# Optimization experiments

Measured on AMD Instinct MI355X. Metric: run time of the kernel, lower is better.

Reference implementation:

```python
import jax, jax.numpy as jnp
import numpy as np
import math

NO, NR, E = 100000, 1000, 1000000
DO, DR, DE, H, OM = 64, 32, 4, 64, 32


def setup_inputs() -> dict:
    key = jax.random.key(0)
    ks = jax.random.split(key, 20)
    s = lambda k, sh: jax.random.normal(k, sh, dtype=jnp.float32) * 0.05
    inp = {
        'x_order': jax.random.normal(ks[0], (NO, DO), dtype=jnp.float32),
        'x_rider': jax.random.normal(ks[1], (NR, DR), dtype=jnp.float32),
        'edge_attr': jax.random.normal(ks[2], (E, DE), dtype=jnp.float32),
        'order_idx': jax.random.randint(ks[3], (E,), 0, NO),
        'rider_idx': jax.random.randint(ks[4], (E,), 0, NR),
        'omega_encoded': jax.random.normal(ks[5], (OM,), dtype=jnp.float32),
        # TransformerConv params (heads=1)
        'Wk': s(ks[6], (DO, H)), 'bk': jnp.zeros((H,), jnp.float32),
        'Wq': s(ks[7], (DR, H)), 'bq': jnp.zeros((H,), jnp.float32),
        'Wv': s(ks[8], (DO, H)), 'bv': jnp.zeros((H,), jnp.float32),
        'We': s(ks[9], (DE, H)),  # lin_edge, bias=False in PyG
        'Wskip': s(ks[10], (DR, H)), 'bskip': jnp.zeros((H,), jnp.float32),
        # order_proj
        'Wp': s(ks[11], (DO, H)), 'bp': jnp.zeros((H,), jnp.float32),
        # residual MLP: Linear(2H+OM,128) -> ReLU -> Linear(128,1)
        'W1': s(ks[12], (2 * H + OM, 128)), 'b1': jnp.zeros((128,), jnp.float32),
        'W2': s(ks[13], (128, 1)), 'b2': jnp.zeros((1,), jnp.float32),
    }
    return inp


def _segment_softmax(alpha, seg, num_segments):
    m = jax.ops.segment_max(alpha, seg, num_segments=num_segments)
    m = jnp.where(jnp.isfinite(m), m, 0.0)
    ex = jnp.exp(alpha - m[seg])
    denom = jax.ops.segment_sum(ex, seg, num_segments=num_segments)
    return ex / (denom[seg] + 1e-16)


def reference(x_order, x_rider, edge_attr, order_idx, rider_idx, omega_encoded,
              Wk, bk, Wq, bq, Wv, bv, We, Wskip, bskip, Wp, bp, W1, b1, W2, b2):
    scale = 1.0 / math.sqrt(H)
    # TransformerConv((order, rider) -> rider), heads=1, edge_dim
    q = x_rider @ Wq + bq            # [NR, H]
    k = x_order @ Wk + bk            # [NO, H]
    v = x_order @ Wv + bv            # [NO, H]
    e = edge_attr @ We               # [E, H]
    k_j = k[order_idx] + e           # [E, H]
    v_j = v[order_idx] + e           # [E, H]
    alpha = jnp.sum(q[rider_idx] * k_j, axis=-1) * scale  # [E]
    alpha = _segment_softmax(alpha, rider_idx, NR)
    agg = jax.ops.segment_sum(alpha[:, None] * v_j, rider_idx, num_segments=NR)  # [NR, H]
    rider_emb = agg + x_rider @ Wskip + bskip  # root/skip connection

    # edge scoring
    order_proj = x_order @ Wp + bp   # [NO, H]
    oe = order_proj[order_idx]       # [E, H]
    re = rider_emb[rider_idx]        # [E, H]
    dot = jnp.sum(oe * re, axis=-1) * scale  # [E]
    omega_expand = jnp.broadcast_to(omega_encoded[None, :], (oe.shape[0], OM))
    resid_in = jnp.concatenate([oe, re, omega_expand], axis=-1)  # [E, 2H+OM]
    hmid = jax.nn.relu(resid_in @ W1 + b1)
    resid = (hmid @ W2 + b2)[:, 0]
    return jnp.clip(dot + resid, -10.0, 10.0)
```

## Files before the change

kernel.cpp:

```cpp
#include <hip/hip_runtime.h>
#include <hip/hip_bf16.h>
#include <math.h>
#include <stdint.h>

#define NO_N 100000
#define NR_N 1000
#define E_N  1000000
#define SB     250
#define SCHUNK 4000
#define KVP_TILES 1563
#define KVP_BLKS 1024
#define MAXTILES 17008

typedef short bf16x8 __attribute__((ext_vector_type(8)));
typedef float floatx4 __attribute__((ext_vector_type(4)));

__device__ __forceinline__ unsigned short bfu(float x) {
    union { __hip_bfloat16 h; unsigned short u; } c;
    c.h = __float2bfloat16(x);
    return c.u;
}
__device__ __forceinline__ float bflo(unsigned int u) {
    return __uint_as_float(u << 16);
}
__device__ __forceinline__ float bfhi(unsigned int u) {
    return __uint_as_float(u & 0xffff0000u);
}

__global__ __launch_bounds__(256) void k_front(
    const float* __restrict__ xr,
    const float* __restrict__ Wq, const float* __restrict__ bq,
    const float* __restrict__ Wskip, const float* __restrict__ bskip,
    const float* __restrict__ We,
    float* __restrict__ q, float* __restrict__ skip, float* __restrict__ t,
    const float* __restrict__ W1, const float* __restrict__ b1,
    const float* __restrict__ omega, float* __restrict__ b1eff,
    const float* __restrict__ x,
    const float* __restrict__ Wk, const float* __restrict__ bk,
    const float* __restrict__ Wv, const float* __restrict__ bv,
    const float* __restrict__ Wp, const float* __restrict__ bp,
    unsigned short* __restrict__ kb, unsigned short* __restrict__ vb,
    unsigned short* __restrict__ pb,
    const int* __restrict__ ridx, int* __restrict__ ghist)
{
    __shared__ __align__(16) char smem[9216];
    const int tid = threadIdx.x;
    const int b = blockIdx.x;

    if (b < 250) {
        float* sx = (float*)smem;
        float* sq = sx + 128;
        int rbase = b * 4;
        if (tid < 128) {
            int rl = tid >> 5, d = tid & 31;
            sx[rl * 32 + d] = xr[(rbase + rl) * 32 + d];
        }
        __syncthreads();
        int rl = tid >> 6, h = tid & 63;
        int r = rbase + rl;
        float aq = bq[h], as = bskip[h];
        #pragma unroll 4
        for (int d = 0; d < 32; ++d) {
            float xv = sx[rl * 32 + d];
            aq += xv * Wq[d * 64 + h];
            as += xv * Wskip[d * 64 + h];
        }
        sq[rl * 64 + h] = aq;
        q[r * 64 + h] = aq;
        skip[r * 64 + h] = as;
        __syncthreads();
        if (tid < 16) {
            int rl2 = tid >> 2, d = tid & 3;
            float acc = 0.f;
            for (int hh = 0; hh < 64; ++hh)
                acc += We[d * 64 + hh] * sq[rl2 * 64 + hh];
            t[(rbase + rl2) * 4 + d] = acc;
        }
    } else if (b == 250) {
        if (tid < 128) {
            float acc = b1[tid];
            #pragma unroll 4
            for (int j = 0; j < 32; ++j)
                acc += omega[j] * W1[(128 + j) * 128 + tid];
            b1eff[tid] = acc;
        }
    } else if (b < 251 + KVP_BLKS) {
        unsigned short* sX = (unsigned short*)smem;
        const int wave = tid >> 6, lane = tid & 63;
        const int l15 = lane & 15, quad = lane >> 4;

        bf16x8 bfr[3][2];
        float bias[3];
        unsigned short* outT[3];
        int colc[3];
        #pragma unroll
        for (int ct = 0; ct < 3; ++ct) {
            int n = wave * 48 + ct * 16 + l15;
            int table = n >> 6, c = n & 63;
            const float* W  = (table == 0) ? Wk : (table == 1) ? Wv : Wp;
            const float* bb = (table == 0) ? bk : (table == 1) ? bv : bp;
            bias[ct] = bb[c];
            colc[ct] = c;
            outT[ct] = (table == 0) ? kb : (table == 1) ? vb : pb;
            #pragma unroll
            for (int kf = 0; kf < 2; ++kf) {
                bf16x8 f;
                #pragma unroll
                for (int j = 0; j < 8; ++j)
                    f[j] = (short)bfu(W[(size_t)(kf * 32 + quad * 8 + j) * 64 + c]);
                bfr[ct][kf] = f;
            }
        }

        const int srl = tid >> 2;
        const int sqt = (tid & 3) * 16;

        for (int tile = b - 251; tile < KVP_TILES; tile += KVP_BLKS) {
            int rowbase = tile * 64;
            {
                int row = rowbase + srl;
                unsigned short* dst = sX + srl * 72 + sqt;
                if (row < NO_N) {
                    const float4* src = (const float4*)(x + (size_t)row * 64 + sqt);
                    #pragma unroll
                    for (int i = 0; i < 4; ++i) {
                        float4 a = src[i];
                        ushort4 u = { bfu(a.x), bfu(a.y), bfu(a.z), bfu(a.w) };
                        *(ushort4*)(dst + i * 4) = u;
                    }
                } else {
                    ushort4 z = {0, 0, 0, 0};
                    #pragma unroll
                    for (int i = 0; i < 4; ++i) *(ushort4*)(dst + i * 4) = z;
                }
            }
            __syncthreads();

            floatx4 acc[4][3];
            #pragma unroll
            for (int rt = 0; rt < 4; ++rt)
                #pragma unroll
                for (int ct = 0; ct < 3; ++ct)
                    acc[rt][ct] = (floatx4){bias[ct], bias[ct], bias[ct], bias[ct]};

            #pragma unroll
            for (int rt = 0; rt < 4; ++rt) {
                const unsigned short* ar = sX + (size_t)(rt * 16 + l15) * 72 + quad * 8;
                bf16x8 a0 = *(const bf16x8*)(ar);
                bf16x8 a1 = *(const bf16x8*)(ar + 32);
                #pragma unroll
                for (int ct = 0; ct < 3; ++ct) {
                    floatx4 c = acc[rt][ct];
                    c = __builtin_amdgcn_mfma_f32_16x16x32_bf16(a0, bfr[ct][0], c, 0, 0, 0);
                    c = __builtin_amdgcn_mfma_f32_16x16x32_bf16(a1, bfr[ct][1], c, 0, 0, 0);
                    acc[rt][ct] = c;
                }
            }

            #pragma unroll
            for (int rt = 0; rt < 4; ++rt) {
                int rb = rowbase + rt * 16 + quad * 4;
                #pragma unroll
                for (int ct = 0; ct < 3; ++ct) {
                    unsigned short* o = outT[ct];
                    size_t cbase = colc[ct];
                    #pragma unroll
                    for (int g = 0; g < 4; ++g) {
                        int row = rb + g;
                        if (row < NO_N)
                            o[(size_t)row * 64 + cbase] = bfu(acc[rt][ct][g]);
                    }
                }
            }
            __syncthreads();
        }
    } else {
        int* hc = (int*)smem;
        int hb = b - (251 + KVP_BLKS);
        for (int i = tid; i < NR_N; i += 256) hc[i] = 0;
        __syncthreads();
        int s = hb * SCHUNK;
        for (int i = s + tid; i < s + SCHUNK; i += 256)
            atomicAdd(&hc[ridx[i]], 1);
        __syncthreads();
        for (int i = tid; i < NR_N; i += 256)
            ghist[i * SB + hb] = hc[i];
    }
}

__global__ __launch_bounds__(256) void k_colscan(const int* __restrict__ ghist,
                                                 int* __restrict__ gpre,
                                                 int* __restrict__ counts)
{
    __shared__ int s[256];
    int tid = threadIdx.x, r = blockIdx.x;
    int v = (tid < SB) ? ghist[r * SB + tid] : 0;
    s[tid] = v;
    __syncthreads();
    for (int off = 1; off < 256; off <<= 1) {
        int tv = (tid >= off) ? s[tid - off] : 0;
        __syncthreads();
        s[tid] += tv;
        __syncthreads();
    }
    if (tid < SB) gpre[r * SB + tid] = s[tid] - v;
    if (tid == 255) counts[r] = s[255];
}

__global__ __launch_bounds__(1024) void k_scan(const int* __restrict__ counts,
                                               int* __restrict__ offsets,
                                               int* __restrict__ tilestart,
                                               int4* __restrict__ trec)
{
    __shared__ int s[1024];
    int tid = threadIdx.x;
    int c = (tid < NR_N) ? counts[tid] : 0;
    s[tid] = c;
    __syncthreads();
    for (int off = 1; off < 1024; off <<= 1) {
        int tv = (tid >= off) ? s[tid - off] : 0;
        __syncthreads();
        s[tid] += tv;
        __syncthreads();
    }
    int off0 = s[tid] - c;
    if (tid < NR_N) offsets[tid] = off0;
    if (tid == NR_N - 1) offsets[NR_N] = s[tid];
    __syncthreads();
    int tc = (tid < NR_N) ? ((c + 63) >> 6) : 0;
    s[tid] = tc;
    __syncthreads();
    for (int off = 1; off < 1024; off <<= 1) {
        int tv = (tid >= off) ? s[tid - off] : 0;
        __syncthreads();
        s[tid] += tv;
        __syncthreads();
    }
    if (tid < NR_N) {
        int ts = s[tid] - tc;
        tilestart[tid] = ts;
        int jend = off0 + c;
        for (int t = 0; t < tc; ++t)
            trec[ts + t] = make_int4(tid, off0 + (t << 6), jend, 0);
    }
    if (tid == NR_N - 1) tilestart[NR_N] = s[tid];
}

__global__ __launch_bounds__(256) void k_scatter2(
    const int* __restrict__ ridx, const int* __restrict__ oidx,
    const float* __restrict__ ea, const float* __restrict__ t,
    const int* __restrict__ offsets, const int* __restrict__ gpre,
    int4* __restrict__ spack, int* __restrict__ so, int* __restrict__ rank)
{
    __shared__ int cur[NR_N];
    int tid = threadIdx.x, b = blockIdx.x;
    for (int i = tid; i < NR_N; i += 256)
        cur[i] = offsets[i] + gpre[i * SB + b];
    __syncthreads();
    int s = b * SCHUNK;
    for (int i = s + tid; i < s + SCHUNK; i += 256) {
        int r = ridx[i];
        int o = oidx[i];
        float4 e4 = *(const float4*)(ea + (size_t)i * 4);
        float4 t4 = *(const float4*)(t + r * 4);
        float h = e4.x * t4.x + e4.y * t4.y + e4.z * t4.z + e4.w * t4.w;
        int pos = atomicAdd(&cur[r], 1);
        int4 pk;
        pk.x = o;
        pk.y = __float_as_int(h);
        pk.z = (int)((unsigned)bfu(e4.x) | ((unsigned)bfu(e4.y) << 16));
        pk.w = (int)((unsigned)bfu(e4.z) | ((unsigned)bfu(e4.w) << 16));
        spack[pos] = pk;
        so[pos] = o;
        rank[i] = pos;
    }
}

__global__ __launch_bounds__(512) void k_rider(
    const int* __restrict__ offsets, const int4* __restrict__ spack,
    const float* __restrict__ q,
    const unsigned short* __restrict__ kb, const unsigned short* __restrict__ vb,
    const float* __restrict__ We, const float* __restrict__ skip,
    const float* __restrict__ W1, const float* __restrict__ b1eff,
    float* __restrict__ emb, float* __restrict__ Br)
{
    __shared__ float sQ[64];
    __shared__ int2 sOX[8][64];
    __shared__ float rv[8][64];
    __shared__ float re4[8][4];
    __shared__ float rd[8];

    int r = blockIdx.x;
    int wave = threadIdx.x >> 6, lane = threadIdx.x & 63;
    if (threadIdx.x < 64) sQ[threadIdx.x] = q[r * 64 + threadIdx.x];
    __syncthreads();

    int beg = offsets[r], end = offsets[r + 1];
    int cnt = end - beg;
    int chunk = (cnt + 7) >> 3;
    int s0 = beg + wave * chunk;
    int s1 = min(s0 + chunk, end);

    float aggv = 0.f, dsum = 0.f;
    float ag0 = 0.f, ag1 = 0.f, ag2 = 0.f, ag3 = 0.f;
    const float2* sQ2 = (const float2*)sQ;

    for (int jb = s0; jb < s1; jb += 64) {
        int j = jb + lane;
        bool valid = (j < s1);
        int4 pk = make_int4(0, 0, 0, 0);
        if (valid) pk = spack[j];
        int oo = pk.x;
        float h = __int_as_float(pk.y);

        const uint4* krow = (const uint4*)(kb + (size_t)oo * 64);
        uint4 K0 = krow[0], K1 = krow[1], K2 = krow[2], K3 = krow[3];
        uint4 K4 = krow[4], K5 = krow[5], K6 = krow[6], K7 = krow[7];
        float acc = h;
        #define DOT8(Kv, base) { \
            float2 qa = sQ2[(base) + 0]; \
            acc = fmaf(bflo(Kv.x), qa.x, acc); acc = fmaf(bfhi(Kv.x), qa.y, acc); \
            float2 qb = sQ2[(base) + 1]; \
            acc = fmaf(bflo(Kv.y), qb.x, acc); acc = fmaf(bfhi(Kv.y), qb.y, acc); \
            float2 qc = sQ2[(base) + 2]; \
            acc = fmaf(bflo(Kv.z), qc.x, acc); acc = fmaf(bfhi(Kv.z), qc.y, acc); \
            float2 qd = sQ2[(base) + 3]; \
            acc = fmaf(bflo(Kv.w), qd.x, acc); acc = fmaf(bfhi(Kv.w), qd.y, acc); }
        DOT8(K0, 0) DOT8(K1, 4) DOT8(K2, 8) DOT8(K3, 12)
        DOT8(K4, 16) DOT8(K5, 20) DOT8(K6, 24) DOT8(K7, 28)
        #undef DOT8

        float exv = valid ? __expf(acc * 0.125f) : 0.f;
        dsum += exv;
        unsigned int ez = (unsigned int)pk.z, ew = (unsigned int)pk.w;
        ag0 = fmaf(exv, bflo(ez), ag0);
        ag1 = fmaf(exv, bfhi(ez), ag1);
        ag2 = fmaf(exv, bflo(ew), ag2);
        ag3 = fmaf(exv, bfhi(ew), ag3);

        sOX[wave][lane] = make_int2(oo, __float_as_int(exv));

        int nn = min(s1 - jb, 64);
        int i = 0;
        for (; i + 8 <= nn; i += 8) {
            int2 x0 = sOX[wave][i + 0], x1 = sOX[wave][i + 1];
            int2 x2 = sOX[wave][i + 2], x3 = sOX[wave][i + 3];
            int2 x4 = sOX[wave][i + 4], x5 = sOX[wave][i + 5];
            int2 x6 = sOX[wave][i + 6], x7 = sOX[wave][i + 7];
            unsigned short u0 = vb[(size_t)x0.x * 64 + lane];
            unsigned short u1 = vb[(size_t)x1.x * 64 + lane];
            unsigned short u2 = vb[(size_t)x2.x * 64 + lane];
            unsigned short u3 = vb[(size_t)x3.x * 64 + lane];
            unsigned short u4 = vb[(size_t)x4.x * 64 + lane];
            unsigned short u5 = vb[(size_t)x5.x * 64 + lane];
            unsigned short u6 = vb[(size_t)x6.x * 64 + lane];
            unsigned short u7 = vb[(size_t)x7.x * 64 + lane];
            aggv = fmaf(__int_as_float(x0.y), __uint_as_float((unsigned int)u0 << 16), aggv);
            aggv = fmaf(__int_as_float(x1.y), __uint_as_float((unsigned int)u1 << 16), aggv);
            aggv = fmaf(__int_as_float(x2.y), __uint_as_float((unsigned int)u2 << 16), aggv);
            aggv = fmaf(__int_as_float(x3.y), __uint_as_float((unsigned int)u3 << 16), aggv);
            aggv = fmaf(__int_as_float(x4.y), __uint_as_float((unsigned int)u4 << 16), aggv);
            aggv = fmaf(__int_as_float(x5.y), __uint_as_float((unsigned int)u5 << 16), aggv);
            aggv = fmaf(__int_as_float(x6.y), __uint_as_float((unsigned int)u6 << 16), aggv);
            aggv = fmaf(__int_as_float(x7.y), __uint_as_float((unsigned int)u7 << 16), aggv);
        }
        for (; i < nn; ++i) {
            int2 xx = sOX[wave][i];
            unsigned short uu = vb[(size_t)xx.x * 64 + lane];
            aggv = fmaf(__int_as_float(xx.y), __uint_as_float((unsigned int)uu << 16), aggv);
        }
    }

    #pragma unroll
    for (int m = 1; m < 64; m <<= 1) {
        dsum += __shfl_xor(dsum, m);
        ag0 += __shfl_xor(ag0, m);
        ag1 += __shfl_xor(ag1, m);
        ag2 += __shfl_xor(ag2, m);
        ag3 += __shfl_xor(ag3, m);
    }

    rv[wave][lane] = aggv;
    if (lane == 0) {
        rd[wave] = dsum;
        re4[wave][0] = ag0; re4[wave][1] = ag1;
        re4[wave][2] = ag2; re4[wave][3] = ag3;
    }
    __syncthreads();
    if (threadIdx.x < 64) {
        int l = threadIdx.x;
        float av = 0.f, ds = 0.f, a0 = 0.f, a1 = 0.f, a2 = 0.f, a3 = 0.f;
        #pragma unroll
        for (int w = 0; w < 8; ++w) {
            av += rv[w][l]; ds += rd[w];
            a0 += re4[w][0]; a1 += re4[w][1]; a2 += re4[w][2]; a3 += re4[w][3];
        }
        float corr = a0 * We[0 * 64 + l] + a1 * We[1 * 64 + l]
                   + a2 * We[2 * 64 + l] + a3 * We[3 * 64 + l];
        float val = (av + corr) / (ds + 1e-16f) + skip[r * 64 + l];
        emb[r * 64 + l] = val;
        sQ[l] = val;
    }
    __syncthreads();
    if (threadIdx.x < 128) {
        int c = threadIdx.x;
        float a = b1eff[c];
        #pragma unroll 8
        for (int d = 0; d < 64; ++d)
            a = fmaf(sQ[d], W1[(size_t)(64 + d) * 128 + c], a);
        Br[r * 128 + c] = a;
    }
}

__global__ __launch_bounds__(256) void k_edge2(
    const int* __restrict__ so, const int4* __restrict__ trec,
    const int* __restrict__ tilestart,
    const unsigned short* __restrict__ pb, const float* __restrict__ emb,
    const float* __restrict__ Br, const float* __restrict__ W1,
    const float* __restrict__ W2, const float* __restrict__ b2,
    float* __restrict__ tmp)
{
    __shared__ __align__(16) unsigned short sA[64 * 72];
    __shared__ float sDot[64];

    const int tid = threadIdx.x;
    const int wave = tid >> 6;
    const int lane = tid & 63;
    const int l15 = lane & 15;
    const int quad = lane >> 4;

    bf16x8 bfr[8][2];
    float w2v[8];
    #pragma unroll
    for (int ctl = 0; ctl < 8; ++ctl) {
        int n = ctl * 16 + l15;
        w2v[ctl] = W2[n];
        #pragma unroll
        for (int kc = 0; kc < 2; ++kc) {
            bf16x8 f;
            #pragma unroll
            for (int j = 0; j < 8; ++j)
                f[j] = (short)bfu(W1[(size_t)(kc * 32 + quad * 8 + j) * 128 + n]);
            bfr[ctl][kc] = f;
        }
    }
    float b2v = b2[0];
    const int ntiles = tilestart[NR_N];
    const int ngrp = (ntiles + 3) >> 2;

    const int el = tid >> 2;
    const int q16 = (tid & 3) * 16;

    for (int g = blockIdx.x; g < ngrp; g += gridDim.x) {
        int tb = g * 4;
        int4 rr[4];
        uint4 P0[4], P1[4];

        #pragma unroll
        for (int i = 0; i < 4; ++i)
            rr[i] = trec[min(tb + i, ntiles - 1)];
        #pragma unroll
        for (int i = 0; i < 4; ++i) {
            int o = so[min(rr[i].y + el, rr[i].z - 1)];
            const uint4* p = (const uint4*)(pb + (size_t)o * 64 + q16);
            P0[i] = p[0];
            P1[i] = p[1];
        }

        #pragma unroll
        for (int i = 0; i < 4; ++i) {
            {
                const float4* pe = (const float4*)(emb + rr[i].x * 64 + q16);
                float4 e0 = pe[0], e1 = pe[1], e2 = pe[2], e3 = pe[3];
                float dotp;
                dotp  = bflo(P0[i].x) * e0.x + bfhi(P0[i].x) * e0.y;
                dotp += bflo(P0[i].y) * e0.z + bfhi(P0[i].y) * e0.w;
                dotp += bflo(P0[i].z) * e1.x + bfhi(P0[i].z) * e1.y;
                dotp += bflo(P0[i].w) * e1.z + bfhi(P0[i].w) * e1.w;
                dotp += bflo(P1[i].x) * e2.x + bfhi(P1[i].x) * e2.y;
                dotp += bflo(P1[i].y) * e2.z + bfhi(P1[i].y) * e2.w;
                dotp += bflo(P1[i].z) * e3.x + bfhi(P1[i].z) * e3.y;
                dotp += bflo(P1[i].w) * e3.z + bfhi(P1[i].w) * e3.w;
                uint4* sp = (uint4*)(sA + el * 72 + q16);
                sp[0] = P0[i]; sp[1] = P1[i];
                dotp += __shfl_xor(dotp, 1);
                dotp += __shfl_xor(dotp, 2);
                if ((tid & 3) == 0) sDot[el] = dotp;
            }
            float brv[8];
            #pragma unroll
            for (int ctl = 0; ctl < 8; ++ctl)
                brv[ctl] = Br[rr[i].x * 128 + ctl * 16 + l15];

            const unsigned short* ar = sA + (size_t)(wave * 16 + l15) * 72 + quad * 8;
            bf16x8 a0 = *(const bf16x8*)(ar);
            bf16x8 a1 = *(const bf16x8*)(ar + 32);
            floatx4 s = (floatx4){0.f, 0.f, 0.f, 0.f};
            #pragma unroll
            for (int ctl = 0; ctl < 8; ++ctl) {
                floatx4 c = (floatx4){0.f, 0.f, 0.f, 0.f};
                c = __builtin_amdgcn_mfma_f32_16x16x32_bf16(a0, bfr[ctl][0], c, 0, 0, 0);
                c = __builtin_amdgcn_mfma_f32_16x16x32_bf16(a1, bfr[ctl][1], c, 0, 0, 0);
                #pragma unroll
                for (int gg = 0; gg < 4; ++gg)
                    s[gg] = fmaf(fmaxf(c[gg] + brv[ctl], 0.f), w2v[ctl], s[gg]);
            }
            #pragma unroll
            for (int m = 1; m < 16; m <<= 1) {
                s[0] += __shfl_xor(s[0], m);
                s[1] += __shfl_xor(s[1], m);
                s[2] += __shfl_xor(s[2], m);
                s[3] += __shfl_xor(s[3], m);
            }
            if (l15 == 0) {
                int rowb = wave * 16 + quad * 4;
                #pragma unroll
                for (int gg = 0; gg < 4; ++gg) {
                    int pos = rr[i].y + rowb + gg;
                    if (pos < rr[i].z) {
                        float v = s[gg] + 0.125f * sDot[rowb + gg] + b2v;
                        tmp[pos] = fminf(fmaxf(v, -10.f), 10.f);
                    }
                }
            }
        }
    }
}

__global__ __launch_bounds__(256) void k_perm(const int* __restrict__ rank,
                                              const float* __restrict__ tmp,
                                              float* __restrict__ out)
{
    int i = blockIdx.x * 256 + threadIdx.x;
    if (i < E_N) out[i] = tmp[rank[i]];
}

extern "C" void kernel_launch(void* const* d_in, const int* in_sizes, int n_in,
                              void* d_out, int out_size, void* d_ws, size_t ws_size,
                              hipStream_t stream)
{
    const float* x_order   = (const float*)d_in[0];
    const float* x_rider   = (const float*)d_in[1];
    const float* edge_attr = (const float*)d_in[2];
    const int*   order_idx = (const int*)d_in[3];
    const int*   rider_idx = (const int*)d_in[4];
    const float* omega     = (const float*)d_in[5];
    const float* Wk = (const float*)d_in[6];  const float* bk = (const float*)d_in[7];
    const float* Wq = (const float*)d_in[8];  const float* bq = (const float*)d_in[9];
    const float* Wv = (const float*)d_in[10]; const float* bv = (const float*)d_in[11];
    const float* We = (const float*)d_in[12];
    const float* Wskip = (const float*)d_in[13]; const float* bskip = (const float*)d_in[14];
    const float* Wp = (const float*)d_in[15]; const float* bp = (const float*)d_in[16];
    const float* W1 = (const float*)d_in[17]; const float* b1 = (const float*)d_in[18];
    const float* W2 = (const float*)d_in[19]; const float* b2 = (const float*)d_in[20];
    float* out = (float*)d_out;

    unsigned short* ws_kb = (unsigned short*)d_ws;
    unsigned short* ws_vb = ws_kb + (size_t)NO_N * 64;
    unsigned short* ws_pb = ws_vb + (size_t)NO_N * 64;
    int4* ws_spack = (int4*)(ws_pb + (size_t)NO_N * 64);
    float* ws_tmp  = (float*)ws_spack;
    int*  ws_so    = (int*)(ws_spack + E_N);
    int*  ws_rank  = ws_so + E_N;
    float* wsf     = (float*)(ws_rank + E_N);
    float* ws_q    = wsf;
    float* ws_skip = ws_q + NR_N * 64;
    float* ws_emb  = ws_skip + NR_N * 64;
    float* ws_t    = ws_emb + NR_N * 64;
    float* ws_b1e  = ws_t + NR_N * 4;
    float* ws_Br   = ws_b1e + 128;
    int* ws_counts  = (int*)(ws_Br + NR_N * 128);
    int* ws_offsets = ws_counts + NR_N;
    int* ws_tilest  = ws_offsets + NR_N + 8;
    int* ws_ghist   = ws_tilest + NR_N + 8;
    int* ws_gpre    = ws_ghist + NR_N * SB;
    int4* ws_trec   = (int4*)(((uintptr_t)(ws_gpre + NR_N * SB) + 15) & ~(uintptr_t)15);

    k_front<<<251 + KVP_BLKS + SB, 256, 0, stream>>>(
        x_rider, Wq, bq, Wskip, bskip, We, ws_q, ws_skip, ws_t,
        W1, b1, omega, ws_b1e,
        x_order, Wk, bk, Wv, bv, Wp, bp, ws_kb, ws_vb, ws_pb,
        rider_idx, ws_ghist);
    k_colscan<<<NR_N, 256, 0, stream>>>(ws_ghist, ws_gpre, ws_counts);
    k_scan<<<1, 1024, 0, stream>>>(ws_counts, ws_offsets, ws_tilest, ws_trec);
    k_scatter2<<<SB, 256, 0, stream>>>(rider_idx, order_idx, edge_attr, ws_t,
                                       ws_offsets, ws_gpre, ws_spack, ws_so, ws_rank);
    k_rider<<<NR_N, 512, 0, stream>>>(ws_offsets, ws_spack, ws_q,
                                      ws_kb, ws_vb, We, ws_skip,
                                      W1, ws_b1e, ws_emb, ws_Br);
    k_edge2<<<4096, 256, 0, stream>>>(ws_so, ws_trec, ws_tilest,
                                      ws_pb, ws_emb, ws_Br, W1, W2, b2, ws_tmp);
    k_perm<<<(E_N + 255) / 256, 256, 0, stream>>>(ws_rank, ws_tmp, out);
}
```

Baseline: 315.4 us.

## Give each wave its own edge tile in k_edge2 and parallelize tile record building

k_edge2 now assigns one 64-edge tile per wave instead of one tile per block. Each lane loads a full 128-byte bf16 projection row and computes the dot product alone, and each wave has a private LDS buffer, so the block-wide synchronization between tiles goes away. k_scan now fills the tile records in parallel with a binary search over tile starts, replacing the serial per-rider loop, and the edge grid is halved. The trade-offs are more registers per lane, four times the LDS, and uncoalesced per-lane row loads and scalar emb reads.

```diff
diff --git a/kernel.cpp b/kernel.cpp
--- a/kernel.cpp
+++ b/kernel.cpp
@@ -213,6 +213,9 @@
                                                int4* __restrict__ trec)
 {
     __shared__ int s[1024];
+    __shared__ int ofsL[NR_N];
+    __shared__ int endL[NR_N];
+    __shared__ int tsL[NR_N + 1];
     int tid = threadIdx.x;
     int c = (tid < NR_N) ? counts[tid] : 0;
     s[tid] = c;
@@ -224,7 +227,11 @@
         __syncthreads();
     }
     int off0 = s[tid] - c;
-    if (tid < NR_N) offsets[tid] = off0;
+    if (tid < NR_N) {
+        offsets[tid] = off0;
+        ofsL[tid] = off0;
+        endL[tid] = off0 + c;
+    }
     if (tid == NR_N - 1) offsets[NR_N] = s[tid];
     __syncthreads();
     int tc = (tid < NR_N) ? ((c + 63) >> 6) : 0;
@@ -238,12 +245,23 @@
     }
     if (tid < NR_N) {
         int ts = s[tid] - tc;
+        tsL[tid] = ts;
         tilestart[tid] = ts;
-        int jend = off0 + c;
-        for (int t = 0; t < tc; ++t)
-            trec[ts + t] = make_int4(tid, off0 + (t << 6), jend, 0);
-    }
-    if (tid == NR_N - 1) tilestart[NR_N] = s[tid];
+    }
+    if (tid == NR_N - 1) {
+        tsL[NR_N] = s[tid];
+        tilestart[NR_N] = s[tid];
+    }
+    __syncthreads();
+    int ntiles = tsL[NR_N];
+    for (int t = tid; t < ntiles; t += 1024) {
+        int lo = 0, hi = NR_N - 1;
+        while (lo < hi) {
+            int mid = (lo + hi + 1) >> 1;
+            if (tsL[mid] <= t) lo = mid; else hi = mid - 1;
+        }
+        trec[t] = make_int4(lo, ofsL[lo] + ((t - tsL[lo]) << 6), endL[lo], 0);
+    }
 }
 
 __global__ __launch_bounds__(256) void k_scatter2(
@@ -420,8 +438,8 @@
     const float* __restrict__ W2, const float* __restrict__ b2,
     float* __restrict__ tmp)
 {
-    __shared__ __align__(16) unsigned short sA[64 * 72];
-    __shared__ float sDot[64];
+    __shared__ __align__(16) unsigned short sA[4][64 * 72];
+    __shared__ float sDot[4][64];
 
     const int tid = threadIdx.x;
     const int wave = tid >> 6;
@@ -446,53 +464,49 @@
     }
     float b2v = b2[0];
     const int ntiles = tilestart[NR_N];
-    const int ngrp = (ntiles + 3) >> 2;
-
-    const int el = tid >> 2;
-    const int q16 = (tid & 3) * 16;
-
-    for (int g = blockIdx.x; g < ngrp; g += gridDim.x) {
-        int tb = g * 4;
-        int4 rr[4];
-        uint4 P0[4], P1[4];
-
+
+    unsigned short* myA = sA[wave];
+    float* myDot = sDot[wave];
+
+    for (int tile = blockIdx.x * 4 + wave; tile < ntiles; tile += gridDim.x * 4) {
+        int4 rr = trec[tile];
+        const int r = rr.x, jb = rr.y, jend = rr.z;
+
+        int o = so[min(jb + lane, jend - 1)];
+        const uint4* prow = (const uint4*)(pb + (size_t)o * 64);
+        uint4 R0 = prow[0], R1 = prow[1], R2 = prow[2], R3 = prow[3];
+        uint4 R4 = prow[4], R5 = prow[5], R6 = prow[6], R7 = prow[7];
+
+        const float* er = emb + r * 64;
+        float dotp = 0.f;
+        #define DOTC(Rv, base) { \
+            dotp = fmaf(bflo(Rv.x), er[(base) + 0], dotp); \
+            dotp = fmaf(bfhi(Rv.x), er[(base) + 1], dotp); \
+            dotp = fmaf(bflo(Rv.y), er[(base) + 2], dotp); \
+            dotp = fmaf(bfhi(Rv.y), er[(base) + 3], dotp); \
+            dotp = fmaf(bflo(Rv.z), er[(base) + 4], dotp); \
+            dotp = fmaf(bfhi(Rv.z), er[(base) + 5], dotp); \
+            dotp = fmaf(bflo(Rv.w), er[(base) + 6], dotp); \
+            dotp = fmaf(bfhi(Rv.w), er[(base) + 7], dotp); }
+        DOTC(R0, 0)  DOTC(R1, 8)  DOTC(R2, 16) DOTC(R3, 24)
+        DOTC(R4, 32) DOTC(R5, 40) DOTC(R6, 48) DOTC(R7, 56)
+        #undef DOTC
+        myDot[lane] = dotp;
+
+        {
+            uint4* dst = (uint4*)(myA + lane * 72);
+            dst[0] = R0; dst[1] = R1; dst[2] = R2; dst[3] = R3;
+            dst[4] = R4; dst[5] = R5; dst[6] = R6; dst[7] = R7;
+        }
+
+        float brv[8];
         #pragma unroll
-        for (int i = 0; i < 4; ++i)
-            rr[i] = trec[min(tb + i, ntiles - 1)];
+        for (int ctl = 0; ctl < 8; ++ctl)
+            brv[ctl] = Br[r * 128 + ctl * 16 + l15];
+
         #pragma unroll
-        for (int i = 0; i < 4; ++i) {
-            int o = so[min(rr[i].y + el, rr[i].z - 1)];
-            const uint4* p = (const uint4*)(pb + (size_t)o * 64 + q16);
-            P0[i] = p[0];
-            P1[i] = p[1];
-        }
-
-        #pragma unroll
-        for (int i = 0; i < 4; ++i) {
-            {
-                const float4* pe = (const float4*)(emb + rr[i].x * 64 + q16);
-                float4 e0 = pe[0], e1 = pe[1], e2 = pe[2], e3 = pe[3];
-                float dotp;
-                dotp  = bflo(P0[i].x) * e0.x + bfhi(P0[i].x) * e0.y;
-                dotp += bflo(P0[i].y) * e0.z + bfhi(P0[i].y) * e0.w;
-                dotp += bflo(P0[i].z) * e1.x + bfhi(P0[i].z) * e1.y;
-                dotp += bflo(P0[i].w) * e1.z + bfhi(P0[i].w) * e1.w;
-                dotp += bflo(P1[i].x) * e2.x + bfhi(P1[i].x) * e2.y;
-                dotp += bflo(P1[i].y) * e2.z + bfhi(P1[i].y) * e2.w;
-                dotp += bflo(P1[i].z) * e3.x + bfhi(P1[i].z) * e3.y;
-                dotp += bflo(P1[i].w) * e3.z + bfhi(P1[i].w) * e3.w;
-                uint4* sp = (uint4*)(sA + el * 72 + q16);
-                sp[0] = P0[i]; sp[1] = P1[i];
-                dotp += __shfl_xor(dotp, 1);
-                dotp += __shfl_xor(dotp, 2);
-                if ((tid & 3) == 0) sDot[el] = dotp;
-            }
-            float brv[8];
-            #pragma unroll
-            for (int ctl = 0; ctl < 8; ++ctl)
-                brv[ctl] = Br[rr[i].x * 128 + ctl * 16 + l15];
-
-            const unsigned short* ar = sA + (size_t)(wave * 16 + l15) * 72 + quad * 8;
+        for (int rt = 0; rt < 4; ++rt) {
+            const unsigned short* ar = myA + (rt * 16 + l15) * 72 + quad * 8;
             bf16x8 a0 = *(const bf16x8*)(ar);
             bf16x8 a1 = *(const bf16x8*)(ar + 32);
             floatx4 s = (floatx4){0.f, 0.f, 0.f, 0.f};
@@ -502,8 +516,8 @@
                 c = __builtin_amdgcn_mfma_f32_16x16x32_bf16(a0, bfr[ctl][0], c, 0, 0, 0);
                 c = __builtin_amdgcn_mfma_f32_16x16x32_bf16(a1, bfr[ctl][1], c, 0, 0, 0);
                 #pragma unroll
-                for (int gg = 0; gg < 4; ++gg)
-                    s[gg] = fmaf(fmaxf(c[gg] + brv[ctl], 0.f), w2v[ctl], s[gg]);
+                for (int g = 0; g < 4; ++g)
+                    s[g] = fmaf(fmaxf(c[g] + brv[ctl], 0.f), w2v[ctl], s[g]);
             }
             #pragma unroll
             for (int m = 1; m < 16; m <<= 1) {
@@ -513,12 +527,12 @@
                 s[3] += __shfl_xor(s[3], m);
             }
             if (l15 == 0) {
-                int rowb = wave * 16 + quad * 4;
+                int rowb = rt * 16 + quad * 4;
                 #pragma unroll
-                for (int gg = 0; gg < 4; ++gg) {
-                    int pos = rr[i].y + rowb + gg;
-                    if (pos < rr[i].z) {
-                        float v = s[gg] + 0.125f * sDot[rowb + gg] + b2v;
+                for (int g = 0; g < 4; ++g) {
+                    int pos = jb + rowb + g;
+                    if (pos < jend) {
+                        float v = s[g] + 0.125f * myDot[rowb + g] + b2v;
                         tmp[pos] = fminf(fmaxf(v, -10.f), 10.f);
                     }
                 }
@@ -588,7 +602,7 @@
     k_rider<<<NR_N, 512, 0, stream>>>(ws_offsets, ws_spack, ws_q,
                                       ws_kb, ws_vb, We, ws_skip,
                                       W1, ws_b1e, ws_emb, ws_Br);
-    k_edge2<<<4096, 256, 0, stream>>>(ws_so, ws_trec, ws_tilest,
+    k_edge2<<<2048, 256, 0, stream>>>(ws_so, ws_trec, ws_tilest,
                                       ws_pb, ws_emb, ws_Br, W1, W2, b2, ws_tmp);
     k_perm<<<(E_N + 255) / 256, 256, 0, stream>>>(ws_rank, ws_tmp, out);
 }
```

Result: no change. 316.7 us (+0.4%).
